# Performance work log

Measured on AMD Instinct MI355X. Metric: run time of the kernel, lower is better.

The kernel has to match this reference:

```python
import jax, jax.numpy as jnp
import numpy as np

N_NODES = 50000
N_EDGES = 300000
F_IN = 11
D = 256


def _gcn_conv(h, src, dst, deg_inv_sqrt, W, b, n):
    """PyG GCNConv: out = D^{-1/2} (A + I) D^{-1/2} (h W) + b.
    src/dst already include self-loops; deg_inv_sqrt precomputed."""
    norm = deg_inv_sqrt[src] * deg_inv_sqrt[dst]          # [E+N]
    hw = h @ W                                            # [N, D]
    msg = hw[src] * norm[:, None]                         # [E+N, D]
    out = jax.ops.segment_sum(msg, dst, num_segments=n)   # [N, D]
    return out + b


def setup_inputs() -> dict:
    key = jax.random.key(0)
    ks = jax.random.split(key, 8)
    x = jax.random.normal(ks[0], (N_NODES, F_IN), dtype=jnp.float32)
    edge_index = jax.random.randint(ks[1], (2, N_EDGES), 0, N_NODES, dtype=jnp.int32)
    s = 0.05
    W_embed = jax.random.normal(ks[2], (F_IN, D), dtype=jnp.float32) * s
    b_embed = jnp.zeros((D,), dtype=jnp.float32)
    W1 = jax.random.normal(ks[3], (D, D), dtype=jnp.float32) * s
    b1 = jnp.zeros((D,), dtype=jnp.float32)
    W2 = jax.random.normal(ks[4], (D, D), dtype=jnp.float32) * s
    b2 = jnp.zeros((D,), dtype=jnp.float32)
    return {"x": x, "edge_index": edge_index, "W_embed": W_embed, "b_embed": b_embed,
            "W1": W1, "b1": b1, "W2": W2, "b2": b2}


def reference(x, edge_index, W_embed, b_embed, W1, b1, W2, b2):
    n = x.shape[0]
    # add self-loops (PyG GCNConv default add_self_loops=True)
    loop = jnp.arange(n, dtype=edge_index.dtype)
    src = jnp.concatenate([edge_index[0], loop])
    dst = jnp.concatenate([edge_index[1], loop])
    # symmetric normalization: deg over target index with unit edge weights
    deg = jax.ops.segment_sum(jnp.ones(src.shape, dtype=x.dtype), dst, num_segments=n)
    deg_inv_sqrt = jnp.where(deg > 0, jax.lax.rsqrt(jnp.maximum(deg, 1e-12)), 0.0)

    h = jax.nn.relu(x @ W_embed + b_embed)                # embed + relu
    h = jax.nn.relu(_gcn_conv(h, src, dst, deg_inv_sqrt, W1, b1, n))
    h = _gcn_conv(h, src, dst, deg_inv_sqrt, W2, b2, n)
    return h
```

## Files before the change

### kernel.cpp

```cpp
#include <hip/hip_runtime.h>

#define N_NODES 50000
#define N_EDGES 300000
#define N_TOT   350000
#define D       256
#define MPAD    50048
#define SCAN_B  196

typedef __attribute__((ext_vector_type(8))) short bf16x8;
typedef __attribute__((ext_vector_type(4))) float f32x4;
typedef __attribute__((ext_vector_type(8))) unsigned short u16x8;

__device__ __forceinline__ float bf2f(unsigned short b) {
    union { unsigned u; float f; } v; v.u = ((unsigned)b) << 16; return v.f;
}
__device__ __forceinline__ unsigned short f2bf(float f) {
    union { float f; unsigned u; } v; v.f = f;
    unsigned u = v.u;
    unsigned r = (u + 0x7FFFu + ((u >> 16) & 1u)) >> 16;
    return (unsigned short)r;
}
__device__ __forceinline__ void g2lds16(const unsigned short* g, unsigned short* l) {
    __builtin_amdgcn_global_load_lds(
        (const __attribute__((address_space(1))) void*)g,
        (__attribute__((address_space(3))) void*)l, 16, 0, 0);
}

__global__ __launch_bounds__(256) void k1_kernel(
        const float* __restrict__ x, const int* __restrict__ ei,
        const float* __restrict__ We, const float* __restrict__ be,
        const float* __restrict__ W1, const float* __restrict__ W2,
        int* __restrict__ cnt,
        unsigned short* __restrict__ Wt1, unsigned short* __restrict__ Wt2,
        unsigned short* __restrict__ hA) {
    int t = threadIdx.x, b = blockIdx.x;
    int tid = b * 256 + t;

    if (tid < N_TOT) {
        int dst = (tid < N_EDGES) ? ei[N_EDGES + tid] : (tid - N_EDGES);
        atomicAdd(&cnt[dst], 1);
    }
    if (tid < 2 * D * D) {
        int wsel = tid >> 16, rem = tid & 65535;
        int tt = rem >> 8, bb = rem & 255;
        const float* W = wsel ? W2 : W1;
        unsigned short* Wt = wsel ? Wt2 : Wt1;
        Wt[bb * D + tt] = f2bf(W[tt * D + bb]);
    }
    float w[11];
    #pragma unroll
    for (int k = 0; k < 11; ++k) w[k] = We[k * D + t];
    float bb = be[t];
    #pragma unroll
    for (int ni = 0; ni < 8; ++ni) {
        int node = b * 8 + ni;
        float acc = 0.f;
        if (node < N_NODES) {
            acc = bb;
            #pragma unroll
            for (int k = 0; k < 11; ++k) acc += x[node * 11 + k] * w[k];
            acc = fmaxf(acc, 0.f);
        }
        hA[(size_t)node * D + t] = f2bf(acc);
    }
}

__global__ void k3_kernel(const int* __restrict__ ei, const int* __restrict__ locs,
                          const int* __restrict__ bsum, const float* __restrict__ dis,
                          int* __restrict__ fc, int* __restrict__ rowptr,
                          int* __restrict__ esrc, float* __restrict__ enorm) {
    int tid = blockIdx.x * 256 + threadIdx.x;
    if (tid == 0) rowptr[0] = 0;
    if (tid < N_NODES)
        rowptr[tid + 1] = locs[tid] + bsum[tid >> 8];
    if (tid < N_TOT) {
        int src, dst;
        if (tid < N_EDGES) { src = ei[tid]; dst = ei[N_EDGES + tid]; }
        else               { src = dst = tid - N_EDGES; }
        int base = bsum[dst >> 8] + ((dst & 255) ? locs[dst - 1] : 0);
        int pos = base + atomicAdd(&fc[dst], 1);
        esrc[pos]  = src;
        enorm[pos] = dis[src] * dis[dst];
    }
}

__global__ __launch_bounds__(256) void gemm_kernel(const unsigned short* __restrict__ A,
                                                   const unsigned short* __restrict__ Bt,
                                                   unsigned short* __restrict__ C,
                                                   const int* __restrict__ cnt,
                                                   float* __restrict__ dis,
                                                   int* __restrict__ locs,
                                                   int* __restrict__ bsum,
                                                   int* __restrict__ done) {
    __shared__ unsigned short lA[128 * 32];
    __shared__ unsigned short lB[128 * 32];
    __shared__ int ws[4];
    __shared__ int amLast;
    int t = threadIdx.x;

    if (cnt && blockIdx.y == 0 && blockIdx.x < SCAN_B) {
        int lane = t & 63, wv4 = t >> 6;
        int i = blockIdx.x * 256 + t;
        int v = (i < N_NODES) ? cnt[i] : 0;
        if (i < N_NODES) dis[i] = rsqrtf((float)v);
        int s = v;
        #pragma unroll
        for (int d = 1; d < 64; d <<= 1) {
            int u = __shfl_up(s, d, 64);
            if (lane >= d) s += u;
        }
        if (lane == 63) ws[wv4] = s;
        __syncthreads();
        int off = 0;
        #pragma unroll
        for (int k = 0; k < 4; ++k) if (k < wv4) off += ws[k];
        s += off;
        if (i < N_NODES) locs[i] = s;
        if (t == 255) {
            bsum[blockIdx.x] = s;
            __threadfence();
            amLast = (atomicAdd(done, 1) == SCAN_B - 1);
        }
        __syncthreads();
        if (amLast) {
            __threadfence();
            int vv = 0;
            if (t < SCAN_B)
                vv = __hip_atomic_load(&bsum[t], __ATOMIC_RELAXED, __HIP_MEMORY_SCOPE_AGENT);
            int ss = vv;
            #pragma unroll
            for (int d = 1; d < 64; d <<= 1) {
                int u = __shfl_up(ss, d, 64);
                if (lane >= d) ss += u;
            }
            __syncthreads();
            if (lane == 63) ws[wv4] = ss;
            __syncthreads();
            int off2 = 0;
            #pragma unroll
            for (int k = 0; k < 4; ++k) if (k < wv4) off2 += ws[k];
            ss += off2;
            if (t < SCAN_B) bsum[t] = ss - vv;
        }
        __syncthreads();
    }

    int wv = t >> 6, lane = t & 63;
    int m0 = blockIdx.x * 128;
    int n0 = blockIdx.y * 128;
    int moff = (wv & 1) * 64, noff = (wv >> 1) * 64;
    int q = lane >> 4, r = lane & 15;

    int srow = t >> 2;
    int skof = (t & 3) * 8;

    const unsigned short* Ag0 = A  + (size_t)(m0 + srow) * D + skof;
    const unsigned short* Ag1 = Ag0 + (size_t)64 * D;
    const unsigned short* Bg0 = Bt + (size_t)(n0 + srow) * D + skof;
    const unsigned short* Bg1 = Bg0 + (size_t)64 * D;
    unsigned short* lA0 = lA + t * 8;
    unsigned short* lA1 = lA0 + 64 * 32;
    unsigned short* lB0 = lB + t * 8;
    unsigned short* lB1 = lB0 + 64 * 32;

    f32x4 acc[4][4] = {};
    for (int kk = 0; kk < D; kk += 32) {
        __syncthreads();
        g2lds16(Ag0 + kk, lA0);
        g2lds16(Ag1 + kk, lA1);
        g2lds16(Bg0 + kk, lB0);
        g2lds16(Bg1 + kk, lB1);
        __syncthreads();
        bf16x8 a[4], b[4];
        #pragma unroll
        for (int mt = 0; mt < 4; ++mt)
            a[mt] = *(const bf16x8*)(lA + (moff + mt * 16 + r) * 32 + q * 8);
        #pragma unroll
        for (int nt = 0; nt < 4; ++nt)
            b[nt] = *(const bf16x8*)(lB + (noff + nt * 16 + r) * 32 + q * 8);
        #pragma unroll
        for (int mt = 0; mt < 4; ++mt)
            #pragma unroll
            for (int nt = 0; nt < 4; ++nt)
                acc[mt][nt] = __builtin_amdgcn_mfma_f32_16x16x32_bf16(a[mt], b[nt], acc[mt][nt], 0, 0, 0);
    }
    #pragma unroll
    for (int mt = 0; mt < 4; ++mt)
        #pragma unroll
        for (int nt = 0; nt < 4; ++nt) {
            int col  = n0 + noff + nt * 16 + r;
            int rowb = m0 + moff + mt * 16 + q * 4;
            #pragma unroll
            for (int i = 0; i < 4; ++i)
                C[(size_t)(rowb + i) * D + col] = f2bf(acc[mt][nt][i]);
        }
}

__global__ __launch_bounds__(256) void agg_kernel(const unsigned short* __restrict__ hw,
                                                  const int* __restrict__ rowptr,
                                                  const int* __restrict__ esrc,
                                                  const float* __restrict__ enorm,
                                                  const float* __restrict__ bias,
                                                  unsigned short* __restrict__ out_bf,
                                                  float* __restrict__ out_f32,
                                                  int mode) {
    int wid  = threadIdx.x >> 6;
    int lane = threadIdx.x & 63;
    int node = blockIdx.x * 4 + wid;
    if (node >= N_NODES) return;
    int s0 = rowptr[node], s1 = rowptr[node + 1];
    int half = lane >> 5, hl = lane & 31;

    float acc[8] = {};
    for (int base = s0; base < s1; base += 64) {
        int ec = s1 - base; if (ec > 64) ec = 64;
        int srcl = 0; float nml = 0.f;
        if (lane < ec) { srcl = esrc[base + lane]; nml = enorm[base + lane]; }
        int it = (ec + 1) >> 1;
        for (int i = 0; i < it; i += 2) {
            int   e0 = (2 * i + half) & 63;
            int   e1 = (2 * i + 2 + half) & 63;
            int   sa = __shfl(srcl, e0, 64);
            float na = __shfl(nml,  e0, 64);
            int   sb = __shfl(srcl, e1, 64);
            float nb = __shfl(nml,  e1, 64);
            u16x8 ha = *(const u16x8*)(hw + (size_t)sa * D + hl * 8);
            u16x8 hb = *(const u16x8*)(hw + (size_t)sb * D + hl * 8);
            #pragma unroll
            for (int k = 0; k < 8; ++k) acc[k] += na * bf2f(ha[k]);
            #pragma unroll
            for (int k = 0; k < 8; ++k) acc[k] += nb * bf2f(hb[k]);
        }
    }
    #pragma unroll
    for (int k = 0; k < 8; ++k) acc[k] += __shfl_xor(acc[k], 32, 64);

    if (lane < 32) {
        int c = hl * 8;
        float4 bv0 = *(const float4*)(bias + c);
        float4 bv1 = *(const float4*)(bias + c + 4);
        float v[8];
        v[0] = acc[0] + bv0.x; v[1] = acc[1] + bv0.y;
        v[2] = acc[2] + bv0.z; v[3] = acc[3] + bv0.w;
        v[4] = acc[4] + bv1.x; v[5] = acc[5] + bv1.y;
        v[6] = acc[6] + bv1.z; v[7] = acc[7] + bv1.w;
        if (mode) {
            u16x8 ov;
            #pragma unroll
            for (int k = 0; k < 8; ++k) ov[k] = f2bf(fmaxf(v[k], 0.f));
            *(u16x8*)(out_bf + (size_t)node * D + c) = ov;
        } else {
            float4 o0 = { v[0], v[1], v[2], v[3] };
            float4 o1 = { v[4], v[5], v[6], v[7] };
            *(float4*)(out_f32 + (size_t)node * D + c)     = o0;
            *(float4*)(out_f32 + (size_t)node * D + c + 4) = o1;
        }
    }
}

extern "C" void kernel_launch(void* const* d_in, const int* in_sizes, int n_in,
                              void* d_out, int out_size, void* d_ws, size_t ws_size,
                              hipStream_t stream) {
    const float* x  = (const float*)d_in[0];
    const int*   ei = (const int*)d_in[1];
    const float* We = (const float*)d_in[2];
    const float* be = (const float*)d_in[3];
    const float* W1 = (const float*)d_in[4];
    const float* b1 = (const float*)d_in[5];
    const float* W2 = (const float*)d_in[6];
    const float* b2 = (const float*)d_in[7];
    float* out = (float*)d_out;

    char* w = (char*)d_ws;
    auto alloc = [&](size_t bytes) {
        char* p = w;
        w += (bytes + 255) & ~(size_t)255;
        return p;
    };
    int*            cnt    = (int*)alloc((size_t)N_NODES * 4);
    int*            fc     = (int*)alloc((size_t)N_NODES * 4);
    int*            done   = (int*)alloc(4);
    size_t zero_span = (size_t)((char*)(done + 64) - (char*)cnt);
    int*            rowptr = (int*)alloc((size_t)(N_NODES + 1) * 4);
    int*            locs   = (int*)alloc((size_t)N_NODES * 4);
    int*            bsum   = (int*)alloc((size_t)SCAN_B * 4);
    float*          dis    = (float*)alloc((size_t)N_NODES * 4);
    int*            esrc   = (int*)alloc((size_t)N_TOT * 4);
    float*          enorm  = (float*)alloc((size_t)N_TOT * 4);
    unsigned short* Wt1    = (unsigned short*)alloc((size_t)D * D * 2);
    unsigned short* Wt2    = (unsigned short*)alloc((size_t)D * D * 2);
    unsigned short* hA     = (unsigned short*)alloc((size_t)MPAD * D * 2);
    unsigned short* hW     = (unsigned short*)alloc((size_t)MPAD * D * 2);

    hipMemsetAsync(cnt, 0, zero_span, stream);
    k1_kernel<<<MPAD / 8, 256, 0, stream>>>(x, ei, We, be, W1, W2, cnt, Wt1, Wt2, hA);

    dim3 ggrid(MPAD / 128, 2);
    gemm_kernel<<<ggrid, 256, 0, stream>>>(hA, Wt1, hW, cnt, dis, locs, bsum, done);
    k3_kernel<<<(N_TOT + 255) / 256, 256, 0, stream>>>(ei, locs, bsum, dis, fc,
                                                       rowptr, esrc, enorm);
    agg_kernel<<<(N_NODES + 3) / 4, 256, 0, stream>>>(hW, rowptr, esrc, enorm, b1,
                                                      hA, nullptr, 1);

    gemm_kernel<<<ggrid, 256, 0, stream>>>(hA, Wt2, hW, nullptr, nullptr, nullptr,
                                           nullptr, nullptr);
    agg_kernel<<<(N_NODES + 3) / 4, 256, 0, stream>>>(hW, rowptr, esrc, enorm, b2,
                                                      nullptr, out, 0);
}
```

Before: 231.5 us.

## Pack edge src/norm, unroll aggregation gather, vectorize GEMM stores, coalesce transpose

Several independent memory-access changes. Edge source index and norm are packed into one int2 array so each edge needs a single 8-byte load. The aggregation inner loop is unrolled to four gathered rows per iteration for more memory-level parallelism. The MFMA operands are swapped so each lane holds four consecutive columns and can write them as one 8-byte store instead of four scattered 2-byte stores. The weight-transpose index mapping is flipped so consecutive threads write consecutive output addresses while their reads become strided. Risks are higher register pressure from the unroll and making sure the swapped-operand output layout stays correct.

```diff
diff --git a/kernel.cpp b/kernel.cpp
--- a/kernel.cpp
+++ b/kernel.cpp
@@ -10,6 +10,7 @@
 typedef __attribute__((ext_vector_type(8))) short bf16x8;
 typedef __attribute__((ext_vector_type(4))) float f32x4;
 typedef __attribute__((ext_vector_type(8))) unsigned short u16x8;
+typedef __attribute__((ext_vector_type(4))) unsigned short u16x4;
 
 __device__ __forceinline__ float bf2f(unsigned short b) {
     union { unsigned u; float f; } v; v.u = ((unsigned)b) << 16; return v.f;
@@ -42,7 +43,7 @@
     }
     if (tid < 2 * D * D) {
         int wsel = tid >> 16, rem = tid & 65535;
-        int tt = rem >> 8, bb = rem & 255;
+        int bb = rem >> 8, tt = rem & 255;
         const float* W = wsel ? W2 : W1;
         unsigned short* Wt = wsel ? Wt2 : Wt1;
         Wt[bb * D + tt] = f2bf(W[tt * D + bb]);
@@ -65,10 +66,11 @@
     }
 }
 
-__global__ void k3_kernel(const int* __restrict__ ei, const int* __restrict__ locs,
+__global__ __launch_bounds__(256) void k3_kernel(const int* __restrict__ ei,
+                          const int* __restrict__ locs,
                           const int* __restrict__ bsum, const float* __restrict__ dis,
                           int* __restrict__ fc, int* __restrict__ rowptr,
-                          int* __restrict__ esrc, float* __restrict__ enorm) {
+                          int2* __restrict__ epk) {
     int tid = blockIdx.x * 256 + threadIdx.x;
     if (tid == 0) rowptr[0] = 0;
     if (tid < N_NODES)
@@ -79,8 +81,7 @@
         else               { src = dst = tid - N_EDGES; }
         int base = bsum[dst >> 8] + ((dst & 255) ? locs[dst - 1] : 0);
         int pos = base + atomicAdd(&fc[dst], 1);
-        esrc[pos]  = src;
-        enorm[pos] = dis[src] * dis[dst];
+        epk[pos] = make_int2(src, __float_as_int(dis[src] * dis[dst]));
     }
 }
 
@@ -182,24 +183,25 @@
         for (int mt = 0; mt < 4; ++mt)
             #pragma unroll
             for (int nt = 0; nt < 4; ++nt)
-                acc[mt][nt] = __builtin_amdgcn_mfma_f32_16x16x32_bf16(a[mt], b[nt], acc[mt][nt], 0, 0, 0);
+                acc[mt][nt] = __builtin_amdgcn_mfma_f32_16x16x32_bf16(b[nt], a[mt], acc[mt][nt], 0, 0, 0);
     }
     #pragma unroll
-    for (int mt = 0; mt < 4; ++mt)
+    for (int mt = 0; mt < 4; ++mt) {
+        int mrow = m0 + moff + mt * 16 + r;
         #pragma unroll
         for (int nt = 0; nt < 4; ++nt) {
-            int col  = n0 + noff + nt * 16 + r;
-            int rowb = m0 + moff + mt * 16 + q * 4;
-            #pragma unroll
-            for (int i = 0; i < 4; ++i)
-                C[(size_t)(rowb + i) * D + col] = f2bf(acc[mt][nt][i]);
-        }
+            int ncol = n0 + noff + nt * 16 + (q << 2);
+            u16x4 o;
+            #pragma unroll
+            for (int i = 0; i < 4; ++i) o[i] = f2bf(acc[mt][nt][i]);
+            *(u16x4*)(C + (size_t)mrow * D + ncol) = o;
+        }
+    }
 }
 
 __global__ __launch_bounds__(256) void agg_kernel(const unsigned short* __restrict__ hw,
                                                   const int* __restrict__ rowptr,
-                                                  const int* __restrict__ esrc,
-                                                  const float* __restrict__ enorm,
+                                                  const int2* __restrict__ epk,
                                                   const float* __restrict__ bias,
                                                   unsigned short* __restrict__ out_bf,
                                                   float* __restrict__ out_f32,
@@ -215,21 +217,36 @@
     for (int base = s0; base < s1; base += 64) {
         int ec = s1 - base; if (ec > 64) ec = 64;
         int srcl = 0; float nml = 0.f;
-        if (lane < ec) { srcl = esrc[base + lane]; nml = enorm[base + lane]; }
+        if (lane < ec) {
+            int2 ep = epk[base + lane];
+            srcl = ep.x; nml = __int_as_float(ep.y);
+        }
         int it = (ec + 1) >> 1;
-        for (int i = 0; i < it; i += 2) {
+        for (int i = 0; i < it; i += 4) {
             int   e0 = (2 * i + half) & 63;
             int   e1 = (2 * i + 2 + half) & 63;
+            int   e2 = (2 * i + 4 + half) & 63;
+            int   e3 = (2 * i + 6 + half) & 63;
             int   sa = __shfl(srcl, e0, 64);
             float na = __shfl(nml,  e0, 64);
             int   sb = __shfl(srcl, e1, 64);
             float nb = __shfl(nml,  e1, 64);
+            int   sc = __shfl(srcl, e2, 64);
+            float nc = __shfl(nml,  e2, 64);
+            int   sd = __shfl(srcl, e3, 64);
+            float nd = __shfl(nml,  e3, 64);
             u16x8 ha = *(const u16x8*)(hw + (size_t)sa * D + hl * 8);
             u16x8 hb = *(const u16x8*)(hw + (size_t)sb * D + hl * 8);
+            u16x8 hc = *(const u16x8*)(hw + (size_t)sc * D + hl * 8);
+            u16x8 hd = *(const u16x8*)(hw + (size_t)sd * D + hl * 8);
             #pragma unroll
             for (int k = 0; k < 8; ++k) acc[k] += na * bf2f(ha[k]);
             #pragma unroll
             for (int k = 0; k < 8; ++k) acc[k] += nb * bf2f(hb[k]);
+            #pragma unroll
+            for (int k = 0; k < 8; ++k) acc[k] += nc * bf2f(hc[k]);
+            #pragma unroll
+            for (int k = 0; k < 8; ++k) acc[k] += nd * bf2f(hd[k]);
         }
     }
     #pragma unroll
@@ -285,8 +302,7 @@
     int*            locs   = (int*)alloc((size_t)N_NODES * 4);
     int*            bsum   = (int*)alloc((size_t)SCAN_B * 4);
     float*          dis    = (float*)alloc((size_t)N_NODES * 4);
-    int*            esrc   = (int*)alloc((size_t)N_TOT * 4);
-    float*          enorm  = (float*)alloc((size_t)N_TOT * 4);
+    int2*           epk    = (int2*)alloc((size_t)N_TOT * 8);
     unsigned short* Wt1    = (unsigned short*)alloc((size_t)D * D * 2);
     unsigned short* Wt2    = (unsigned short*)alloc((size_t)D * D * 2);
     unsigned short* hA     = (unsigned short*)alloc((size_t)MPAD * D * 2);
@@ -298,12 +314,12 @@
     dim3 ggrid(MPAD / 128, 2);
     gemm_kernel<<<ggrid, 256, 0, stream>>>(hA, Wt1, hW, cnt, dis, locs, bsum, done);
     k3_kernel<<<(N_TOT + 255) / 256, 256, 0, stream>>>(ei, locs, bsum, dis, fc,
-                                                       rowptr, esrc, enorm);
-    agg_kernel<<<(N_NODES + 3) / 4, 256, 0, stream>>>(hW, rowptr, esrc, enorm, b1,
+                                                       rowptr, epk);
+    agg_kernel<<<(N_NODES + 3) / 4, 256, 0, stream>>>(hW, rowptr, epk, b1,
                                                       hA, nullptr, 1);
 
     gemm_kernel<<<ggrid, 256, 0, stream>>>(hA, Wt2, hW, nullptr, nullptr, nullptr,
                                            nullptr, nullptr);
-    agg_kernel<<<(N_NODES + 3) / 4, 256, 0, stream>>>(hW, rowptr, esrc, enorm, b2,
+    agg_kernel<<<(N_NODES + 3) / 4, 256, 0, stream>>>(hW, rowptr, epk, b2,
                                                       nullptr, out, 0);
 }
```

Measured after the change: 240.1 us. 1.04x slower.
